# Optimization experiments

Hardware: AMD Instinct MI355X
Metric: run time of the kernel (lower is better)

The kernel has to match this reference:

```python
import jax, jax.numpy as jnp
import numpy as np

B, L = 4, 1024
D_MODEL, D_STATE, N_LAYERS, EXPAND = 512, 16, 4, 2
ED = EXPAND * D_MODEL            # 1024
DT_RANK = -(-D_MODEL // 16)       # ceil(d_model/16) = 32
D_CONV = 4
N_IN, N_OUT, N_FUT = 3, 2, 10
EPS = 1e-5


def setup_inputs() -> dict:
    key = jax.random.key(0)
    ks = jax.random.split(key, 16)
    s = 0.05
    inp = {
        "temporal_seq": jax.random.normal(ks[0], (B, L, N_IN), jnp.float32),
        # input / output projections (torch Linear: weight [out,in])
        "Wi": jax.random.normal(ks[1], (D_MODEL, N_IN), jnp.float32) * s,
        "bi": jnp.zeros((D_MODEL,), jnp.float32),
        "Wo": jax.random.normal(ks[2], (N_FUT * N_OUT, D_MODEL), jnp.float32) * s,
        "bo": jnp.zeros((N_FUT * N_OUT,), jnp.float32),
        # final LayerNorm
        "ln_g": jnp.ones((D_MODEL,), jnp.float32),
        "ln_b": jnp.zeros((D_MODEL,), jnp.float32),
        # stacked per-layer MambaBlock params
        "lWin": jax.random.normal(ks[3], (N_LAYERS, 2 * ED, D_MODEL), jnp.float32) * s,
        "lconvw": jax.random.normal(ks[4], (N_LAYERS, ED, 1, D_CONV), jnp.float32) * 0.2,
        "lconvb": jnp.zeros((N_LAYERS, ED), jnp.float32),
        "lWx": jax.random.normal(ks[5], (N_LAYERS, DT_RANK + 2 * D_STATE, ED), jnp.float32) * s,
        "lWdt": jax.random.normal(ks[6], (N_LAYERS, ED, DT_RANK), jnp.float32) * s,
        "lbdt": jnp.full((N_LAYERS, ED), -3.0, jnp.float32),  # small initial dt
        "lAlog": jnp.log(jnp.broadcast_to(jnp.arange(1.0, D_STATE + 1.0, dtype=jnp.float32), (N_LAYERS, ED, D_STATE))),
        "lD": jnp.ones((N_LAYERS, ED), jnp.float32),
        "lWout": jax.random.normal(ks[7], (N_LAYERS, D_MODEL, ED), jnp.float32) * s,
    }
    return inp


def _scan_op(l, r):
    al, bl = l
    ar, br = r
    return al * ar, ar * bl + br


def _mamba_block(x, Win, convw, convb, Wx, Wdt, bdt, Alog, Dp, Wout):
    # x: [B, L, D_MODEL]
    xz = jnp.einsum("bld,ed->ble", x, Win)          # [B, L, 2*ED]
    xb, z = jnp.split(xz, 2, axis=-1)
    # causal depthwise conv1d (padding d_conv-1 on the left == torch pad+trim)
    xc = jnp.transpose(xb, (0, 2, 1))                 # [B, ED, L]
    xc = jax.lax.conv_general_dilated(xc, convw, (1,), [(D_CONV - 1, 0)], feature_group_count=ED)
    xb = jnp.transpose(xc + convb[None, :, None], (0, 2, 1))
    xb = jax.nn.silu(xb)                              # [B, L, ED]
    # SSM parameters
    dbc = jnp.einsum("ble,fe->blf", xb, Wx)          # [B, L, DT_RANK+2N]
    delta = jax.nn.softplus(dbc[..., :DT_RANK] @ Wdt.T + bdt)   # [B, L, ED]
    Bm = dbc[..., DT_RANK:DT_RANK + D_STATE]          # [B, L, N]
    Cm = dbc[..., DT_RANK + D_STATE:]                 # [B, L, N]
    A = -jnp.exp(Alog)                                # [ED, N]
    dA = jnp.exp(delta[..., None] * A)                # [B, L, ED, N]
    dBx = (delta * xb)[..., None] * Bm[:, :, None, :] # [B, L, ED, N]
    # parallel associative scan: h_t = dA_t * h_{t-1} + dBx_t
    _, hs = jax.lax.associative_scan(_scan_op, (dA, dBx), axis=1)
    y = jnp.einsum("blen,bln->ble", hs, Cm) + Dp * xb
    y = y * jax.nn.silu(z)
    return jnp.einsum("ble,de->bld", y, Wout)


def reference(temporal_seq, Wi, bi, Wo, bo, ln_g, ln_b, lWin, lconvw, lconvb, lWx, lWdt, lbdt, lAlog, lD, lWout):
    x = temporal_seq @ Wi.T + bi                      # [B, L, D_MODEL]
    for i in range(N_LAYERS):
        x = _mamba_block(x, lWin[i], lconvw[i], lconvb[i], lWx[i], lWdt[i], lbdt[i], lAlog[i], lD[i], lWout[i])
    mu = jnp.mean(x, axis=-1, keepdims=True)
    var = jnp.mean((x - mu) ** 2, axis=-1, keepdims=True)
    x = (x - mu) / jnp.sqrt(var + EPS) * ln_g + ln_b
    h_final = x[:, -1, :]                             # [B, D_MODEL]
    u = h_final @ Wo.T + bo                           # [B, N_FUT*N_OUT]
    return u.reshape(-1, N_FUT, N_OUT)
```

## Files before the change

### kernel.cpp

```cpp
#include <hip/hip_runtime.h>
#include <hip/hip_bf16.h>
#include <math.h>

constexpr int Bx = 4, Lx = 1024, DM = 512, DS = 16, NL = 4, EDx = 1024;
constexpr int DTR = 32;

typedef __attribute__((ext_vector_type(8))) short short8v;
typedef __attribute__((ext_vector_type(4))) short short4v;
typedef __attribute__((ext_vector_type(4))) float f32x4;

__device__ inline short f2bf(float f) {
  union { __hip_bfloat16 h; short s; } u;
  u.h = __float2bfloat16(f);
  return u.s;
}
__device__ inline float bf2f(short s) {
  union { __hip_bfloat16 h; short s; } u;
  u.s = s;
  return __bfloat162float(u.h);
}
__device__ inline void store8(short* p, short8v v) {
  *(short4v*)(p)     = __builtin_shufflevector(v, v, 0, 1, 2, 3);
  *(short4v*)(p + 4) = __builtin_shufflevector(v, v, 4, 5, 6, 7);
}

__global__ __launch_bounds__(256) void k_init_x(const float* __restrict__ seq,
    const float* __restrict__ Wi, const float* __restrict__ bi, float* __restrict__ x) {
  int idx = blockIdx.x * 256 + threadIdx.x;
  int d = idx & (DM - 1);
  int bl = idx >> 9;
  float s0 = seq[bl * 3 + 0], s1 = seq[bl * 3 + 1], s2 = seq[bl * 3 + 2];
  x[idx] = bi[d] + s0 * Wi[d * 3 + 0] + s1 * Wi[d * 3 + 1] + s2 * Wi[d * 3 + 2];
}

__global__ __launch_bounds__(256) void k_split(const float* __restrict__ s,
    short* __restrict__ hi, short* __restrict__ lo) {
  int i = blockIdx.x * 256 + threadIdx.x;
  const float4 v = ((const float4*)s)[i];
  short4v h, l;
  h.x = f2bf(v.x); l.x = f2bf(v.x - bf2f(h.x));
  h.y = f2bf(v.y); l.y = f2bf(v.y - bf2f(h.y));
  h.z = f2bf(v.z); l.z = f2bf(v.z - bf2f(h.z));
  h.w = f2bf(v.w); l.w = f2bf(v.w - bf2f(h.w));
  ((short4v*)hi)[i] = h;
  ((short4v*)lo)[i] = l;
}

template <int BM, int BN>
__global__ __launch_bounds__(256) void k_gemm_bfp(
    const short* __restrict__ Ahg, const short* __restrict__ Alg,
    const short* __restrict__ Bhg, const short* __restrict__ Blg,
    float* __restrict__ C, int ldc, int K) {
  constexpr int MR = BM / 32, NR = BN / 32;
  __shared__ short Ah[BM][44], Al[BM][44], Bh[BN][44], Bl[BN][44];
  const int tid = threadIdx.x;
  const int w = tid >> 6, lane = tid & 63;
  const int wr = w >> 1, wc = w & 1;
  const int r16 = lane & 15, kh = lane >> 4;
  const int m0 = blockIdx.x * BM, n0 = blockIdx.y * BN;

  f32x4 acc[MR][NR];
  #pragma unroll
  for (int i = 0; i < MR; ++i)
    #pragma unroll
    for (int j = 0; j < NR; ++j) {
      acc[i][j][0] = 0.f; acc[i][j][1] = 0.f; acc[i][j][2] = 0.f; acc[i][j][3] = 0.f;
    }

  for (int k0 = 0; k0 < K; k0 += 32) {
    __syncthreads();
    #pragma unroll
    for (int p = 0; p < BM / 64; ++p) {
      int f = tid + p * 256;
      int r = f >> 2, c8 = (f & 3) << 3;
      size_t g = (size_t)(m0 + r) * K + k0 + c8;
      store8(&Ah[r][c8], *(const short8v*)(Ahg + g));
      store8(&Al[r][c8], *(const short8v*)(Alg + g));
    }
    #pragma unroll
    for (int p = 0; p < BN / 64; ++p) {
      int f = tid + p * 256;
      int r = f >> 2, c8 = (f & 3) << 3;
      size_t g = (size_t)(n0 + r) * K + k0 + c8;
      store8(&Bh[r][c8], *(const short8v*)(Bhg + g));
      store8(&Bl[r][c8], *(const short8v*)(Blg + g));
    }
    __syncthreads();
    short8v ah[MR], al[MR], bh[NR], bl[NR];
    #pragma unroll
    for (int i = 0; i < MR; ++i) {
      int rr = wr * (BM / 2) + i * 16 + r16;
      ah[i] = *(const short8v*)(&Ah[rr][kh * 8]);
      al[i] = *(const short8v*)(&Al[rr][kh * 8]);
    }
    #pragma unroll
    for (int j = 0; j < NR; ++j) {
      int cc = wc * (BN / 2) + j * 16 + r16;
      bh[j] = *(const short8v*)(&Bh[cc][kh * 8]);
      bl[j] = *(const short8v*)(&Bl[cc][kh * 8]);
    }
    #pragma unroll
    for (int i = 0; i < MR; ++i)
      #pragma unroll
      for (int j = 0; j < NR; ++j) {
        acc[i][j] = __builtin_amdgcn_mfma_f32_16x16x32_bf16(ah[i], bh[j], acc[i][j], 0, 0, 0);
        acc[i][j] = __builtin_amdgcn_mfma_f32_16x16x32_bf16(ah[i], bl[j], acc[i][j], 0, 0, 0);
        acc[i][j] = __builtin_amdgcn_mfma_f32_16x16x32_bf16(al[i], bh[j], acc[i][j], 0, 0, 0);
      }
  }
  #pragma unroll
  for (int i = 0; i < MR; ++i) {
    int row_base = m0 + wr * (BM / 2) + i * 16 + kh * 4;
    #pragma unroll
    for (int j = 0; j < NR; ++j) {
      int col = n0 + wc * (BN / 2) + j * 16 + r16;
      #pragma unroll
      for (int r = 0; r < 4; ++r)
        C[(size_t)(row_base + r) * ldc + col] = acc[i][j][r];
    }
  }
}

template <int SK>
__global__ __launch_bounds__(256) void k_xproj_mfma(
    const float* __restrict__ A,
    const float* __restrict__ W,
    float* __restrict__ PART) {
  constexpr int BM = 128, BN = 64, KS = 1024 / SK;
  constexpr int MR = 4, NR = 2;
  __shared__ short Ah[BM][44], Al[BM][44], Bh[BN][44], Bl[BN][44];
  const int tid = threadIdx.x;
  const int w = tid >> 6, lane = tid & 63;
  const int wr = w >> 1, wc = w & 1;
  const int r16 = lane & 15, kh = lane >> 4;
  const int m0 = blockIdx.x * BM;
  const int kbeg = blockIdx.z * KS;

  f32x4 acc[MR][NR];
  #pragma unroll
  for (int i = 0; i < MR; ++i)
    #pragma unroll
    for (int j = 0; j < NR; ++j) {
      acc[i][j][0] = 0.f; acc[i][j][1] = 0.f; acc[i][j][2] = 0.f; acc[i][j][3] = 0.f;
    }

  for (int k0 = kbeg; k0 < kbeg + KS; k0 += 32) {
    __syncthreads();
    #pragma unroll
    for (int p = 0; p < BM / 32; ++p) {
      int f = tid + p * 256;
      int r = f >> 3, c = (f & 7) << 2;
      const float4 v = *(const float4*)(A + (size_t)(m0 + r) * 1024 + k0 + c);
      short h0 = f2bf(v.x), h1 = f2bf(v.y), h2 = f2bf(v.z), h3 = f2bf(v.w);
      Ah[r][c + 0] = h0; Ah[r][c + 1] = h1; Ah[r][c + 2] = h2; Ah[r][c + 3] = h3;
      Al[r][c + 0] = f2bf(v.x - bf2f(h0));
      Al[r][c + 1] = f2bf(v.y - bf2f(h1));
      Al[r][c + 2] = f2bf(v.z - bf2f(h2));
      Al[r][c + 3] = f2bf(v.w - bf2f(h3));
    }
    #pragma unroll
    for (int p = 0; p < BN / 32; ++p) {
      int f = tid + p * 256;
      int r = f >> 3, c = (f & 7) << 2;
      const float4 v = *(const float4*)(W + (size_t)r * 1024 + k0 + c);
      short h0 = f2bf(v.x), h1 = f2bf(v.y), h2 = f2bf(v.z), h3 = f2bf(v.w);
      Bh[r][c + 0] = h0; Bh[r][c + 1] = h1; Bh[r][c + 2] = h2; Bh[r][c + 3] = h3;
      Bl[r][c + 0] = f2bf(v.x - bf2f(h0));
      Bl[r][c + 1] = f2bf(v.y - bf2f(h1));
      Bl[r][c + 2] = f2bf(v.z - bf2f(h2));
      Bl[r][c + 3] = f2bf(v.w - bf2f(h3));
    }
    __syncthreads();
    short8v ah[MR], al[MR], bh[NR], bl[NR];
    #pragma unroll
    for (int i = 0; i < MR; ++i) {
      int rr = wr * 64 + i * 16 + r16;
      ah[i] = *(const short8v*)(&Ah[rr][kh * 8]);
      al[i] = *(const short8v*)(&Al[rr][kh * 8]);
    }
    #pragma unroll
    for (int j = 0; j < NR; ++j) {
      int cc = wc * 32 + j * 16 + r16;
      bh[j] = *(const short8v*)(&Bh[cc][kh * 8]);
      bl[j] = *(const short8v*)(&Bl[cc][kh * 8]);
    }
    #pragma unroll
    for (int i = 0; i < MR; ++i)
      #pragma unroll
      for (int j = 0; j < NR; ++j) {
        acc[i][j] = __builtin_amdgcn_mfma_f32_16x16x32_bf16(ah[i], bh[j], acc[i][j], 0, 0, 0);
        acc[i][j] = __builtin_amdgcn_mfma_f32_16x16x32_bf16(ah[i], bl[j], acc[i][j], 0, 0, 0);
        acc[i][j] = __builtin_amdgcn_mfma_f32_16x16x32_bf16(al[i], bh[j], acc[i][j], 0, 0, 0);
      }
  }
  float* Cp = PART + (size_t)blockIdx.z * (4096 * 64);
  #pragma unroll
  for (int i = 0; i < MR; ++i) {
    int row_base = m0 + wr * 64 + i * 16 + kh * 4;
    #pragma unroll
    for (int j = 0; j < NR; ++j) {
      int col = wc * 32 + j * 16 + r16;
      #pragma unroll
      for (int r = 0; r < 4; ++r)
        Cp[(size_t)(row_base + r) * 64 + col] = acc[i][j][r];
    }
  }
}

template <int SK>
__global__ __launch_bounds__(256) void k_redux(const float* __restrict__ PART,
                                               float* __restrict__ out) {
  int i = blockIdx.x * 256 + threadIdx.x;
  float4 s = ((const float4*)PART)[i];
  #pragma unroll
  for (int k = 1; k < SK; ++k) {
    const float4 v = ((const float4*)PART)[i + k * 65536];
    s.x += v.x; s.y += v.y; s.z += v.z; s.w += v.w;
  }
  ((float4*)out)[i] = s;
}

template <int BM, int BN, int EPI>
__global__ __launch_bounds__(256) void k_gemm_tn(
    const float* __restrict__ A, int lda,
    const float* __restrict__ W, int ldw,
    const float* __restrict__ bias,
    float* __restrict__ C, int ldc, int K) {
  constexpr int BK = 16;
  constexpr int MR = BM / 16, NR = BN / 16;
  __shared__ float As[BK][BM + 4];
  __shared__ float Bs[BK][BN + 4];
  const int tid = threadIdx.x;
  const int tx = tid & 15, ty = tid >> 4;
  const int m0 = blockIdx.x * BM, n0 = blockIdx.y * BN;
  const int arow = tid >> 2;
  const int akol = (tid & 3) << 2;
  float acc[MR][NR] = {};
  for (int k0 = 0; k0 < K; k0 += BK) {
    #pragma unroll
    for (int r = 0; r < BM / 64; ++r) {
      int m = arow + r * 64;
      const float4 v = *(const float4*)(A + (size_t)(m0 + m) * lda + k0 + akol);
      As[akol + 0][m] = v.x; As[akol + 1][m] = v.y;
      As[akol + 2][m] = v.z; As[akol + 3][m] = v.w;
    }
    if constexpr (BN >= 64) {
      #pragma unroll
      for (int r = 0; r < BN / 64; ++r) {
        int n = arow + r * 64;
        const float4 v = *(const float4*)(W + (size_t)(n0 + n) * ldw + k0 + akol);
        Bs[akol + 0][n] = v.x; Bs[akol + 1][n] = v.y;
        Bs[akol + 2][n] = v.z; Bs[akol + 3][n] = v.w;
      }
    } else {
      if (arow < BN) {
        const float4 v = *(const float4*)(W + (size_t)(n0 + arow) * ldw + k0 + akol);
        Bs[akol + 0][arow] = v.x; Bs[akol + 1][arow] = v.y;
        Bs[akol + 2][arow] = v.z; Bs[akol + 3][arow] = v.w;
      }
    }
    __syncthreads();
    #pragma unroll
    for (int k = 0; k < BK; ++k) {
      float af[MR], bf[NR];
      #pragma unroll
      for (int i = 0; i < MR; ++i) af[i] = As[k][ty * MR + i];
      #pragma unroll
      for (int j = 0; j < NR; ++j) bf[j] = Bs[k][tx * NR + j];
      #pragma unroll
      for (int i = 0; i < MR; ++i)
        #pragma unroll
        for (int j = 0; j < NR; ++j)
          acc[i][j] = fmaf(af[i], bf[j], acc[i][j]);
    }
    __syncthreads();
  }
  #pragma unroll
  for (int i = 0; i < MR; ++i) {
    int m = m0 + ty * MR + i;
    #pragma unroll
    for (int j = 0; j < NR; ++j) {
      int n = n0 + tx * NR + j;
      float v = acc[i][j];
      if constexpr (EPI == 1) {
        v += bias[n];
        v = (v > 20.f) ? v : log1pf(__expf(v));
      }
      C[(size_t)m * ldc + n] = v;
    }
  }
}

__global__ __launch_bounds__(256) void k_conv_silu4(const float* __restrict__ xz,
    const float* __restrict__ cw, const float* __restrict__ cb, float* __restrict__ xb) {
  int idx = blockIdx.x * 256 + threadIdx.x;
  int e4 = (idx & 255) << 2;
  int bl = idx >> 8;
  int l = bl & (Lx - 1);
  const float4 w0 = ((const float4*)cw)[e4 + 0];
  const float4 w1 = ((const float4*)cw)[e4 + 1];
  const float4 w2 = ((const float4*)cw)[e4 + 2];
  const float4 w3 = ((const float4*)cw)[e4 + 3];
  float4 acc = ((const float4*)cb)[idx & 255];
  const float* base = xz + (size_t)bl * (2 * EDx) + e4;
  if (l >= 3) { const float4 x = *(const float4*)(base - 3 * 2 * EDx);
    acc.x = fmaf(x.x, w0.x, acc.x); acc.y = fmaf(x.y, w1.x, acc.y);
    acc.z = fmaf(x.z, w2.x, acc.z); acc.w = fmaf(x.w, w3.x, acc.w); }
  if (l >= 2) { const float4 x = *(const float4*)(base - 2 * 2 * EDx);
    acc.x = fmaf(x.x, w0.y, acc.x); acc.y = fmaf(x.y, w1.y, acc.y);
    acc.z = fmaf(x.z, w2.y, acc.z); acc.w = fmaf(x.w, w3.y, acc.w); }
  if (l >= 1) { const float4 x = *(const float4*)(base - 1 * 2 * EDx);
    acc.x = fmaf(x.x, w0.z, acc.x); acc.y = fmaf(x.y, w1.z, acc.y);
    acc.z = fmaf(x.z, w2.z, acc.z); acc.w = fmaf(x.w, w3.z, acc.w); }
  { const float4 x = *(const float4*)(base);
    acc.x = fmaf(x.x, w0.w, acc.x); acc.y = fmaf(x.y, w1.w, acc.y);
    acc.z = fmaf(x.z, w2.w, acc.z); acc.w = fmaf(x.w, w3.w, acc.w); }
  acc.x /= (1.f + __expf(-acc.x));
  acc.y /= (1.f + __expf(-acc.y));
  acc.z /= (1.f + __expf(-acc.z));
  acc.w /= (1.f + __expf(-acc.w));
  ((float4*)xb)[idx] = acc;
}

#define CVT4(V) { V.x = -__expf(V.x) * 1.44269504f; V.y = -__expf(V.y) * 1.44269504f; \
                  V.z = -__expf(V.z) * 1.44269504f; V.w = -__expf(V.w) * 1.44269504f; }

#define ST4PQ(Av, Pv, Qv, Bv) { \
  float a0 = exp2f(dl * Av.x); Pv.x *= a0; Qv.x = fmaf(a0, Qv.x, dx * Bv.x); \
  float a1 = exp2f(dl * Av.y); Pv.y *= a1; Qv.y = fmaf(a1, Qv.y, dx * Bv.y); \
  float a2 = exp2f(dl * Av.z); Pv.z *= a2; Qv.z = fmaf(a2, Qv.z, dx * Bv.z); \
  float a3 = exp2f(dl * Av.w); Pv.w *= a3; Qv.w = fmaf(a3, Qv.w, dx * Bv.w); }

#define ST4Y(Av, Hv, Bv, Cv) { \
  float a0 = exp2f(dl * Av.x); Hv.x = fmaf(a0, Hv.x, dx * Bv.x); y = fmaf(Hv.x, Cv.x, y); \
  float a1 = exp2f(dl * Av.y); Hv.y = fmaf(a1, Hv.y, dx * Bv.y); y = fmaf(Hv.y, Cv.y, y); \
  float a2 = exp2f(dl * Av.z); Hv.z = fmaf(a2, Hv.z, dx * Bv.z); y = fmaf(Hv.z, Cv.z, y); \
  float a3 = exp2f(dl * Av.w); Hv.w = fmaf(a3, Hv.w, dx * Bv.w); y = fmaf(Hv.w, Cv.w, y); }

template <int NCt>
__global__ __launch_bounds__(256) void k_scan1(
    const float* __restrict__ del, const float* __restrict__ xb,
    const float* __restrict__ dbc, const float* __restrict__ Alog,
    float* __restrict__ PQ) {
  constexpr int CTt = Lx / NCt;
  const int idx = blockIdx.x * 256 + threadIdx.x;
  const int ch = idx & 4095, c = idx >> 12;
  const int b = ch >> 10, e = ch & 1023;
  float4 A0, A1, A2, A3;
  {
    const float4* ar = (const float4*)(Alog + e * DS);
    A0 = ar[0]; A1 = ar[1]; A2 = ar[2]; A3 = ar[3];
    CVT4(A0); CVT4(A1); CVT4(A2); CVT4(A3);
  }
  float4 P0 = {1,1,1,1}, P1 = {1,1,1,1}, P2 = {1,1,1,1}, P3 = {1,1,1,1};
  float4 Q0 = {0,0,0,0}, Q1 = {0,0,0,0}, Q2 = {0,0,0,0}, Q3 = {0,0,0,0};
  const size_t bl0 = (size_t)b * Lx + c * CTt;
  const float* dp  = del + bl0 * EDx + e;
  const float* xp  = xb  + bl0 * EDx + e;
  const float* bcp = dbc + bl0 * 64 + 32;
  #pragma unroll 2
  for (int i = 0; i < CTt; ++i) {
    float dl = dp[0];
    float xbl = xp[0];
    float dx = dl * xbl;
    const float4* bp = (const float4*)bcp;
    float4 B0 = bp[0], B1 = bp[1], B2 = bp[2], B3 = bp[3];
    ST4PQ(A0, P0, Q0, B0); ST4PQ(A1, P1, Q1, B1);
    ST4PQ(A2, P2, Q2, B2); ST4PQ(A3, P3, Q3, B3);
    dp += EDx; xp += EDx; bcp += 64;
  }
  float4* o = (float4*)(PQ + (size_t)idx * 32);
  o[0] = P0; o[1] = P1; o[2] = P2; o[3] = P3;
  o[4] = Q0; o[5] = Q1; o[6] = Q2; o[7] = Q3;
}

template <int NCt>
__global__ __launch_bounds__(256) void k_scan2(float* __restrict__ PQ) {
  const int idx = blockIdx.x * 256 + threadIdx.x;
  const int ch = idx >> 4, n = idx & 15;
  constexpr int G = 8;
  const size_t off = (size_t)ch * 32 + n;
  float Pa[G], Qa[G], Pb[G], Qb[G];
  #pragma unroll
  for (int j = 0; j < G; ++j) {
    size_t base = (size_t)j * (4096 * 32) + off;
    Pa[j] = PQ[base]; Qa[j] = PQ[base + 16];
  }
  float H = 0.f;
  #pragma unroll
  for (int gp = 0; gp < NCt / (2 * G); ++gp) {
    const int cA = 2 * gp * G, cB = (2 * gp + 1) * G, cN = (2 * gp + 2) * G;
    #pragma unroll
    for (int j = 0; j < G; ++j) {
      size_t base = (size_t)(cB + j) * (4096 * 32) + off;
      Pb[j] = PQ[base]; Qb[j] = PQ[base + 16];
    }
    #pragma unroll
    for (int j = 0; j < G; ++j) {
      size_t base = (size_t)(cA + j) * (4096 * 32) + off;
      PQ[base + 16] = H;
      H = fmaf(Pa[j], H, Qa[j]);
    }
    if (gp + 1 < NCt / (2 * G)) {
      #pragma unroll
      for (int j = 0; j < G; ++j) {
        size_t base = (size_t)(cN + j) * (4096 * 32) + off;
        Pa[j] = PQ[base]; Qa[j] = PQ[base + 16];
      }
    }
    #pragma unroll
    for (int j = 0; j < G; ++j) {
      size_t base = (size_t)(cB + j) * (4096 * 32) + off;
      PQ[base + 16] = H;
      H = fmaf(Pb[j], H, Qb[j]);
    }
  }
}

template <int NCt>
__global__ __launch_bounds__(256) void k_scan3(
    float* __restrict__ dy,
    const float* __restrict__ xb,
    const float* __restrict__ dbc,
    const float* __restrict__ xz,
    const float* __restrict__ Alog, const float* __restrict__ Dp,
    const float* __restrict__ PQ) {
  constexpr int CTt = Lx / NCt;
  const int idx = blockIdx.x * 256 + threadIdx.x;
  const int ch = idx & 4095, c = idx >> 12;
  const int b = ch >> 10, e = ch & 1023;
  float4 A0, A1, A2, A3;
  {
    const float4* ar = (const float4*)(Alog + e * DS);
    A0 = ar[0]; A1 = ar[1]; A2 = ar[2]; A3 = ar[3];
    CVT4(A0); CVT4(A1); CVT4(A2); CVT4(A3);
  }
  float4 H0, H1, H2, H3;
  {
    const float4* hi = (const float4*)(PQ + (size_t)idx * 32 + 16);
    H0 = hi[0]; H1 = hi[1]; H2 = hi[2]; H3 = hi[3];
  }
  const float De = Dp[e];
  const size_t bl0 = (size_t)b * Lx + c * CTt;
  float* dyp = dy + bl0 * EDx + e;
  const float* xp  = xb + bl0 * EDx + e;
  const float* bcp = dbc + bl0 * 64 + 32;
  const float* zp  = xz + bl0 * (2 * EDx) + EDx + e;
  #pragma unroll 2
  for (int i = 0; i < CTt; ++i) {
    float dl = dyp[0];
    float xbl = xp[0];
    float zv = zp[0];
    float dx = dl * xbl;
    const float4* bp = (const float4*)bcp;
    float4 B0 = bp[0], B1 = bp[1], B2 = bp[2], B3 = bp[3];
    float4 C0 = bp[4], C1 = bp[5], C2 = bp[6], C3 = bp[7];
    float y = 0.f;
    ST4Y(A0, H0, B0, C0); ST4Y(A1, H1, B1, C1);
    ST4Y(A2, H2, B2, C2); ST4Y(A3, H3, B3, C3);
    y = fmaf(De, xbl, y);
    y *= zv / (1.f + __expf(-zv));
    dyp[0] = y;
    dyp += EDx; xp += EDx; bcp += 64; zp += 2 * EDx;
  }
}

__global__ __launch_bounds__(256) void k_ln_head(
    const float* __restrict__ x, const float* __restrict__ g,
    const float* __restrict__ be, const float* __restrict__ Wo,
    const float* __restrict__ bo, float* __restrict__ out) {
  const int b = blockIdx.x;
  const int t = threadIdx.x;
  const float* xr = x + ((size_t)b * Lx + (Lx - 1)) * DM;
  __shared__ float w1[4], w2[4];
  __shared__ float xn[DM];
  __shared__ float hp[20][8];
  float a0 = xr[t], a1 = xr[t + 256];
  float p = a0 + a1;
  #pragma unroll
  for (int o = 32; o > 0; o >>= 1) p += __shfl_down(p, o);
  if ((t & 63) == 0) w1[t >> 6] = p;
  __syncthreads();
  float mean = (w1[0] + w1[1] + w1[2] + w1[3]) * (1.f / DM);
  float d0 = a0 - mean, d1 = a1 - mean;
  p = d0 * d0 + d1 * d1;
  #pragma unroll
  for (int o = 32; o > 0; o >>= 1) p += __shfl_down(p, o);
  if ((t & 63) == 0) w2[t >> 6] = p;
  __syncthreads();
  float rstd = rsqrtf((w2[0] + w2[1] + w2[2] + w2[3]) * (1.f / DM) + 1e-5f);
  xn[t] = d0 * rstd * g[t] + be[t];
  xn[t + 256] = d1 * rstd * g[t + 256] + be[t + 256];
  __syncthreads();
  if (t < 160) {
    int j = t / 8, sg = t % 8;
    const float* wr = Wo + (size_t)j * DM + sg * 64;
    const float* xs = xn + sg * 64;
    float s = 0.f;
    #pragma unroll
    for (int k = 0; k < 64; ++k) s = fmaf(xs[k], wr[k], s);
    hp[j][sg] = s;
  }
  __syncthreads();
  if (t < 20) {
    float s = bo[t];
    #pragma unroll
    for (int k = 0; k < 8; ++k) s += hp[t][k];
    out[b * 20 + t] = s;
  }
}

extern "C" void kernel_launch(void* const* d_in, const int* in_sizes, int n_in,
                              void* d_out, int out_size, void* d_ws, size_t ws_size,
                              hipStream_t stream) {
  (void)in_sizes; (void)n_in; (void)out_size;
  const float* seq    = (const float*)d_in[0];
  const float* Wi     = (const float*)d_in[1];
  const float* bi     = (const float*)d_in[2];
  const float* Wo     = (const float*)d_in[3];
  const float* bo     = (const float*)d_in[4];
  const float* ln_g   = (const float*)d_in[5];
  const float* ln_b   = (const float*)d_in[6];
  const float* lWin   = (const float*)d_in[7];
  const float* lconvw = (const float*)d_in[8];
  const float* lconvb = (const float*)d_in[9];
  const float* lWx    = (const float*)d_in[10];
  const float* lWdt   = (const float*)d_in[11];
  const float* lbdt   = (const float*)d_in[12];
  const float* lAlog  = (const float*)d_in[13];
  const float* lD     = (const float*)d_in[14];
  const float* lWout  = (const float*)d_in[15];

  float* ws  = (float*)d_ws;
  float* X   = ws;
  float* XZ  = X + 2097152;
  float* XB  = XZ + 8388608;
  float* DBC = XB + 4194304;
  float* DEL = DBC + 262144;
  float* PQ  = DEL + 4194304;

  short* PQs   = (short*)PQ;
  short* Xh    = PQs;
  short* Xl    = PQs + 2097152;
  short* Winh  = PQs + 4194304;
  short* Winl  = PQs + 5242880;
  short* Yh    = PQs;
  short* Yl    = PQs + 4194304;
  short* Wouth = PQs + 8388608;
  short* Woutl = PQs + 8912896;
  float* PART  = PQ;

  const bool nc128 = ws_size >= (size_t)143654912;

  k_init_x<<<dim3(Bx * Lx * DM / 256), 256, 0, stream>>>(seq, Wi, bi, X);

  for (int i = 0; i < NL; ++i) {
    const float* Win  = lWin   + (size_t)i * 2048 * 512;
    const float* cw   = lconvw + (size_t)i * EDx * 4;
    const float* cb   = lconvb + (size_t)i * EDx;
    const float* Wx   = lWx    + (size_t)i * 64 * EDx;
    const float* Wdt  = lWdt   + (size_t)i * EDx * DTR;
    const float* bdt  = lbdt   + (size_t)i * EDx;
    const float* Alog = lAlog  + (size_t)i * EDx * DS;
    const float* Dp   = lD     + (size_t)i * EDx;
    const float* Wout = lWout  + (size_t)i * DM * EDx;

    k_split<<<dim3(2048), 256, 0, stream>>>(X, Xh, Xl);
    k_split<<<dim3(1024), 256, 0, stream>>>(Win, Winh, Winl);
    k_gemm_bfp<128, 128><<<dim3(32, 16), 256, 0, stream>>>(Xh, Xl, Winh, Winl, XZ, 2 * EDx, DM);
    k_conv_silu4<<<dim3(Bx * Lx * EDx / 1024), 256, 0, stream>>>(XZ, cw, cb, XB);
    k_xproj_mfma<8><<<dim3(32, 1, 8), 256, 0, stream>>>(XB, Wx, PART);
    k_redux<8><<<dim3(256), 256, 0, stream>>>(PART, DBC);
    k_gemm_tn<128, 64, 1><<<dim3(32, 16), 256, 0, stream>>>(DBC, 64, Wdt, DTR, bdt, DEL, EDx, DTR);
    if (nc128) {
      k_scan1<128><<<dim3(4096 * 128 / 256), 256, 0, stream>>>(DEL, XB, DBC, Alog, PQ);
      k_scan2<128><<<dim3(4096 * DS / 256), 256, 0, stream>>>(PQ);
      k_scan3<128><<<dim3(4096 * 128 / 256), 256, 0, stream>>>(DEL, XB, DBC, XZ, Alog, Dp, PQ);
    } else {
      k_scan1<64><<<dim3(4096 * 64 / 256), 256, 0, stream>>>(DEL, XB, DBC, Alog, PQ);
      k_scan2<64><<<dim3(4096 * DS / 256), 256, 0, stream>>>(PQ);
      k_scan3<64><<<dim3(4096 * 64 / 256), 256, 0, stream>>>(DEL, XB, DBC, XZ, Alog, Dp, PQ);
    }
    k_split<<<dim3(4096), 256, 0, stream>>>(DEL, Yh, Yl);
    k_split<<<dim3(512), 256, 0, stream>>>(Wout, Wouth, Woutl);
    k_gemm_bfp<128, 64><<<dim3(32, 8), 256, 0, stream>>>(Yh, Yl, Wouth, Woutl, X, DM, EDx);
  }

  k_ln_head<<<dim3(Bx), 256, 0, stream>>>(X, ln_g, ln_b, Wo, bo, (float*)d_out);
}
```

Baseline: 966.1 us.

## Fuse bf16 hi/lo splitting into producer kernels and drop split launches

Activation hi/lo bf16 splits are now written directly by the producers (init, out-projection GEMM epilogue, scan3 output) instead of separate k_split passes over X and the scan output. This removes two full read/write sweeps of large activation buffers per layer. The workspace is relaid out so the split buffers no longer alias PQ, which lowers the scan chunk count (128→64 or 64→32 chunks) and reduces scan parallelism. That is a possible loss.

```diff
diff --git a/kernel.cpp b/kernel.cpp
--- a/kernel.cpp
+++ b/kernel.cpp
@@ -25,12 +25,17 @@
 }
 
 __global__ __launch_bounds__(256) void k_init_x(const float* __restrict__ seq,
-    const float* __restrict__ Wi, const float* __restrict__ bi, float* __restrict__ x) {
+    const float* __restrict__ Wi, const float* __restrict__ bi,
+    float* __restrict__ x, short* __restrict__ xh, short* __restrict__ xl) {
   int idx = blockIdx.x * 256 + threadIdx.x;
   int d = idx & (DM - 1);
   int bl = idx >> 9;
   float s0 = seq[bl * 3 + 0], s1 = seq[bl * 3 + 1], s2 = seq[bl * 3 + 2];
-  x[idx] = bi[d] + s0 * Wi[d * 3 + 0] + s1 * Wi[d * 3 + 1] + s2 * Wi[d * 3 + 2];
+  float v = bi[d] + s0 * Wi[d * 3 + 0] + s1 * Wi[d * 3 + 1] + s2 * Wi[d * 3 + 2];
+  x[idx] = v;
+  short h = f2bf(v);
+  xh[idx] = h;
+  xl[idx] = f2bf(v - bf2f(h));
 }
 
 __global__ __launch_bounds__(256) void k_split(const float* __restrict__ s,
@@ -46,11 +51,12 @@
   ((short4v*)lo)[i] = l;
 }
 
-template <int BM, int BN>
+template <int BM, int BN, bool WPAIR>
 __global__ __launch_bounds__(256) void k_gemm_bfp(
     const short* __restrict__ Ahg, const short* __restrict__ Alg,
     const short* __restrict__ Bhg, const short* __restrict__ Blg,
-    float* __restrict__ C, int ldc, int K) {
+    float* __restrict__ C, short* __restrict__ Ch, short* __restrict__ Cl,
+    int ldc, int K) {
   constexpr int MR = BM / 32, NR = BN / 32;
   __shared__ short Ah[BM][44], Al[BM][44], Bh[BN][44], Bl[BN][44];
   const int tid = threadIdx.x;
@@ -115,8 +121,16 @@
     for (int j = 0; j < NR; ++j) {
       int col = n0 + wc * (BN / 2) + j * 16 + r16;
       #pragma unroll
-      for (int r = 0; r < 4; ++r)
-        C[(size_t)(row_base + r) * ldc + col] = acc[i][j][r];
+      for (int r = 0; r < 4; ++r) {
+        float v = acc[i][j][r];
+        size_t o = (size_t)(row_base + r) * ldc + col;
+        C[o] = v;
+        if constexpr (WPAIR) {
+          short h = f2bf(v);
+          Ch[o] = h;
+          Cl[o] = f2bf(v - bf2f(h));
+        }
+      }
     }
   }
 }
@@ -419,12 +433,13 @@
 
 template <int NCt>
 __global__ __launch_bounds__(256) void k_scan3(
-    float* __restrict__ dy,
+    const float* __restrict__ del,
     const float* __restrict__ xb,
     const float* __restrict__ dbc,
     const float* __restrict__ xz,
     const float* __restrict__ Alog, const float* __restrict__ Dp,
-    const float* __restrict__ PQ) {
+    const float* __restrict__ PQ,
+    short* __restrict__ yh, short* __restrict__ yl) {
   constexpr int CTt = Lx / NCt;
   const int idx = blockIdx.x * 256 + threadIdx.x;
   const int ch = idx & 4095, c = idx >> 12;
@@ -442,10 +457,12 @@
   }
   const float De = Dp[e];
   const size_t bl0 = (size_t)b * Lx + c * CTt;
-  float* dyp = dy + bl0 * EDx + e;
+  const float* dyp = del + bl0 * EDx + e;
   const float* xp  = xb + bl0 * EDx + e;
   const float* bcp = dbc + bl0 * 64 + 32;
   const float* zp  = xz + bl0 * (2 * EDx) + EDx + e;
+  short* yhp = yh + bl0 * EDx + e;
+  short* ylp = yl + bl0 * EDx + e;
   #pragma unroll 2
   for (int i = 0; i < CTt; ++i) {
     float dl = dyp[0];
@@ -460,8 +477,10 @@
     ST4Y(A2, H2, B2, C2); ST4Y(A3, H3, B3, C3);
     y = fmaf(De, xbl, y);
     y *= zv / (1.f + __expf(-zv));
-    dyp[0] = y;
-    dyp += EDx; xp += EDx; bcp += 64; zp += 2 * EDx;
+    short h = f2bf(y);
+    yhp[0] = h;
+    ylp[0] = f2bf(y - bf2f(h));
+    dyp += EDx; xp += EDx; bcp += 64; zp += 2 * EDx; yhp += EDx; ylp += EDx;
   }
 }
 
@@ -538,21 +557,22 @@
   float* DBC = XB + 4194304;
   float* DEL = DBC + 262144;
   float* PQ  = DEL + 4194304;
-
-  short* PQs   = (short*)PQ;
-  short* Xh    = PQs;
-  short* Xl    = PQs + 2097152;
-  short* Winh  = PQs + 4194304;
-  short* Winl  = PQs + 5242880;
-  short* Yh    = PQs;
-  short* Yl    = PQs + 4194304;
-  short* Wouth = PQs + 8388608;
-  short* Woutl = PQs + 8912896;
-  float* PART  = PQ;
-
-  const bool nc128 = ws_size >= (size_t)143654912;
-
-  k_init_x<<<dim3(Bx * Lx * DM / 256), 256, 0, stream>>>(seq, Wi, bi, X);
+  float* PART = PQ;
+
+  const bool nc64 = ws_size >= (size_t)141557760;
+  const int  pqf  = nc64 ? 8388608 : 4194304;
+
+  short* S     = (short*)(PQ + pqf);
+  short* Xh    = S;
+  short* Xl    = S + 2097152;
+  short* Yh    = S + 4194304;
+  short* Yl    = S + 8388608;
+  short* Winh  = S + 12582912;
+  short* Winl  = S + 13631488;
+  short* Wouth = S + 14680064;
+  short* Woutl = S + 15204352;
+
+  k_init_x<<<dim3(Bx * Lx * DM / 256), 256, 0, stream>>>(seq, Wi, bi, X, Xh, Xl);
 
   for (int i = 0; i < NL; ++i) {
     const float* Win  = lWin   + (size_t)i * 2048 * 512;
@@ -565,25 +585,25 @@
     const float* Dp   = lD     + (size_t)i * EDx;
     const float* Wout = lWout  + (size_t)i * DM * EDx;
 
-    k_split<<<dim3(2048), 256, 0, stream>>>(X, Xh, Xl);
     k_split<<<dim3(1024), 256, 0, stream>>>(Win, Winh, Winl);
-    k_gemm_bfp<128, 128><<<dim3(32, 16), 256, 0, stream>>>(Xh, Xl, Winh, Winl, XZ, 2 * EDx, DM);
+    k_gemm_bfp<128, 128, false><<<dim3(32, 16), 256, 0, stream>>>(
+        Xh, Xl, Winh, Winl, XZ, nullptr, nullptr, 2 * EDx, DM);
     k_conv_silu4<<<dim3(Bx * Lx * EDx / 1024), 256, 0, stream>>>(XZ, cw, cb, XB);
     k_xproj_mfma<8><<<dim3(32, 1, 8), 256, 0, stream>>>(XB, Wx, PART);
     k_redux<8><<<dim3(256), 256, 0, stream>>>(PART, DBC);
     k_gemm_tn<128, 64, 1><<<dim3(32, 16), 256, 0, stream>>>(DBC, 64, Wdt, DTR, bdt, DEL, EDx, DTR);
-    if (nc128) {
-      k_scan1<128><<<dim3(4096 * 128 / 256), 256, 0, stream>>>(DEL, XB, DBC, Alog, PQ);
-      k_scan2<128><<<dim3(4096 * DS / 256), 256, 0, stream>>>(PQ);
-      k_scan3<128><<<dim3(4096 * 128 / 256), 256, 0, stream>>>(DEL, XB, DBC, XZ, Alog, Dp, PQ);
-    } else {
+    if (nc64) {
       k_scan1<64><<<dim3(4096 * 64 / 256), 256, 0, stream>>>(DEL, XB, DBC, Alog, PQ);
       k_scan2<64><<<dim3(4096 * DS / 256), 256, 0, stream>>>(PQ);
-      k_scan3<64><<<dim3(4096 * 64 / 256), 256, 0, stream>>>(DEL, XB, DBC, XZ, Alog, Dp, PQ);
-    }
-    k_split<<<dim3(4096), 256, 0, stream>>>(DEL, Yh, Yl);
+      k_scan3<64><<<dim3(4096 * 64 / 256), 256, 0, stream>>>(DEL, XB, DBC, XZ, Alog, Dp, PQ, Yh, Yl);
+    } else {
+      k_scan1<32><<<dim3(4096 * 32 / 256), 256, 0, stream>>>(DEL, XB, DBC, Alog, PQ);
+      k_scan2<32><<<dim3(4096 * DS / 256), 256, 0, stream>>>(PQ);
+      k_scan3<32><<<dim3(4096 * 32 / 256), 256, 0, stream>>>(DEL, XB, DBC, XZ, Alog, Dp, PQ, Yh, Yl);
+    }
     k_split<<<dim3(512), 256, 0, stream>>>(Wout, Wouth, Woutl);
-    k_gemm_bfp<128, 64><<<dim3(32, 8), 256, 0, stream>>>(Yh, Yl, Wouth, Woutl, X, DM, EDx);
+    k_gemm_bfp<128, 64, true><<<dim3(32, 8), 256, 0, stream>>>(
+        Yh, Yl, Wouth, Woutl, X, Xh, Xl, DM, EDx);
   }
 
   k_ln_head<<<dim3(Bx), 256, 0, stream>>>(X, ln_g, ln_b, Wo, bo, (float*)d_out);
```

After: 945.1 us. 2.2% less time.
